# Kernel optimization log

Measured on AMD Instinct MI355X. Metric: run time of the kernel, lower is better.

## Reference

```python
import jax, jax.numpy as jnp
import numpy as np

B, L, D, Z, V, N, MAXPOS = 8, 2048, 1024, 128, 2048, 16, 2048


def setup_inputs():
    key = jax.random.key(0)
    ks = jax.random.split(key, 16)
    std = 0.02
    return {
        "x": jax.random.normal(ks[0], (B, L, D), jnp.float32),
        "norm1_w": jnp.ones((D,), jnp.float32),
        "norm1_b": jnp.zeros((D,), jnp.float32),
        "ema_delta": jax.random.normal(ks[1], (D, N), jnp.float32) * 0.2,
        "ema_alpha": jax.random.normal(ks[2], (D, N), jnp.float32) * 0.2,
        "ema_beta": jax.random.normal(ks[3], (D, N), jnp.float32) * 0.02,
        "ema_gamma": jax.random.normal(ks[4], (D, N), jnp.float32),
        "ema_omega": jax.random.normal(ks[5], (D,), jnp.float32),
        "vproj_w": jax.random.normal(ks[6], (D, V), jnp.float32) * std,
        "vproj_b": jnp.zeros((V,), jnp.float32),
        "mx_w": jax.random.normal(ks[7], (D, Z + V + 2 * D), jnp.float32) * std,
        "mx_b": jnp.zeros((Z + V + 2 * D,), jnp.float32),
        "h_w": jax.random.normal(ks[8], (V, D), jnp.float32) * std,
        "h_b": jnp.zeros((D,), jnp.float32),
        "att_gamma": jax.random.normal(ks[9], (2, Z), jnp.float32) * std,
        "att_beta": jnp.zeros((2, Z), jnp.float32),
        "rel_bias": jax.random.normal(ks[10], (2 * MAXPOS - 1,), jnp.float32) * std,
        "norm2_w": jnp.ones((D,), jnp.float32),
        "norm2_b": jnp.zeros((D,), jnp.float32),
        "ff_w1": jax.random.normal(ks[11], (D, 2 * D), jnp.float32) * std,
        "ff_b1": jnp.zeros((2 * D,), jnp.float32),
        "ff_w2": jax.random.normal(ks[12], (2 * D, D), jnp.float32) * std,
        "ff_b2": jnp.zeros((D,), jnp.float32),
    }


def _layernorm(x, w, b):
    mu = jnp.mean(x, -1, keepdims=True)
    var = jnp.mean((x - mu) ** 2, -1, keepdims=True)
    return (x - mu) * jax.lax.rsqrt(var + 1e-5) * w + b


def reference(x, norm1_w, norm1_b, ema_delta, ema_alpha, ema_beta, ema_gamma, ema_omega,
              vproj_w, vproj_b, mx_w, mx_b, h_w, h_b, att_gamma, att_beta, rel_bias,
              norm2_w, norm2_b, ff_w1, ff_b1, ff_w2, ff_b2):
    residual = x
    xn = _layernorm(x, norm1_w, norm1_b)                       # prenorm
    v = jax.nn.silu(xn @ vproj_w + vproj_b)                    # (B L V)

    # --- MultiHeadEMA (damped EMA state space) via FFT convolution ---
    p = jax.nn.sigmoid(ema_delta)                              # (D N)
    q = 1.0 - p * jax.nn.sigmoid(ema_alpha)                    # (D N) in (0,1)
    t = jnp.arange(L, dtype=jnp.float32)
    vander = jnp.exp(t[None, None, :] * jnp.log(q)[:, :, None])       # (D N L)
    kern = jnp.einsum('dnl,dn->dl', (p * ema_beta)[:, :, None] * vander,
                      ema_gamma * np.float32(1.0 / np.sqrt(N)))        # (D L)
    xT = jnp.swapaxes(xn, 1, 2)                                # (B D L)
    k_f = jnp.fft.rfft(kern, n=2 * L)
    x_f = jnp.fft.rfft(xT, n=2 * L)
    ema = jnp.fft.irfft(x_f * k_f, n=2 * L)[..., :L]           # causal conv
    mx = jax.nn.silu(jnp.swapaxes(ema, 1, 2) + xn * ema_omega) # (B L D)

    # --- moving-average gated attention ---
    base = mx @ mx_w + mx_b                                    # (B L D+Z+V+D)
    u, zr, hx = jnp.split(base, [D, D + Z + V], axis=-1)
    u = jax.nn.sigmoid(u)                                      # update gate
    zr = jax.nn.silu(zr)
    z, r = zr[..., :Z], zr[..., Z:]                            # (B L Z), (B L V)
    zqk = z[:, :, None, :] * att_gamma + att_beta              # (B L 2 Z)
    qh, kh = zqk[:, :, 0, :], zqk[:, :, 1, :]

    # simple relative positional bias: Toeplitz bias[i,j] = b[L-1 + j - i]
    bseg = rel_bias[MAXPOS - L:MAXPOS + L - 1]                 # (2L-1,)
    idx = (L - 1) + jnp.arange(L)[None, :] - jnp.arange(L)[:, None]
    bias = bseg[idx]                                           # (L L)

    qk = jnp.einsum('blz,bmz->blm', qh * np.float32(Z ** -0.5), kh) + bias
    attn = jax.nn.softmax(qk, axis=-1)                         # (B L L)
    h = jnp.einsum('blm,bmv->blv', attn, v)                    # (B L V)
    h = jax.nn.silu(hx + (h * r) @ h_w + h_b)                  # (B L D)
    out = residual + u * (h - residual)                        # addcmul gate

    # --- prenorm FFN residual block (expand=2, silu) ---
    y = _layernorm(out, norm2_w, norm2_b)
    y = jax.nn.silu(y @ ff_w1 + ff_b1) @ ff_w2 + ff_b2
    return out + y
```

## Files before the change

kernel.cpp:

```cpp
#include <hip/hip_runtime.h>
#include <hip/hip_bf16.h>
#include <cstdint>

#define B_ 8
#define L_ 2048
#define D_ 1024
#define Z_ 128
#define V_ 2048
#define N_ 16
#define NC_ 16
#define CL_ 128

typedef unsigned short ushort_t;
typedef __attribute__((ext_vector_type(8))) short short8;
typedef __attribute__((ext_vector_type(4))) float floatx4;

__device__ __forceinline__ float b2f(ushort_t u){ union{float f;unsigned i;}x; x.i=((unsigned)u)<<16; return x.f; }
__device__ __forceinline__ ushort_t f2b(float f){ union{float f;unsigned i;}x; x.f=f; unsigned r=(x.i+0x7fffu+((x.i>>16)&1u))>>16; return (ushort_t)r; }
__device__ __forceinline__ float sigmoidf_(float x){ return 1.0f/(1.0f+__expf(-x)); }
__device__ __forceinline__ float siluf_(float x){ return x/(1.0f+__expf(-x)); }

#define GLL16(g,l) __builtin_amdgcn_global_load_lds( \
    (const __attribute__((address_space(1))) void*)(g), \
    (__attribute__((address_space(3))) void*)(l), 16, 0, 0)

__device__ __forceinline__ float blockSum(float v){
  #pragma unroll
  for(int off=32;off;off>>=1) v += __shfl_xor(v,off);
  __shared__ float sm[4];
  __syncthreads();
  if((threadIdx.x&63)==0) sm[threadIdx.x>>6]=v;
  __syncthreads();
  return (sm[0]+sm[1])+(sm[2]+sm[3]);
}
__device__ __forceinline__ float blockMax(float v){
  #pragma unroll
  for(int off=32;off;off>>=1) v = fmaxf(v,__shfl_xor(v,off));
  __shared__ float sm[4];
  __syncthreads();
  if((threadIdx.x&63)==0) sm[threadIdx.x>>6]=v;
  __syncthreads();
  return fmaxf(fmaxf(sm[0],sm[1]),fmaxf(sm[2],sm[3]));
}

__global__ __launch_bounds__(256) void ln_kernel(const float* __restrict__ in,
    const float* __restrict__ w, const float* __restrict__ b,
    ushort_t* __restrict__ o16){
  const int row = blockIdx.x;
  const int t = threadIdx.x;
  const float* p = in + (size_t)row*D_;
  float4 v = *reinterpret_cast<const float4*>(p + t*4);
  float s = (v.x+v.y)+(v.z+v.w);
  s = blockSum(s);
  float mu = s*(1.0f/D_);
  float dx=v.x-mu, dy=v.y-mu, dz=v.z-mu, dw=v.w-mu;
  float ss = dx*dx+dy*dy+dz*dz+dw*dw;
  ss = blockSum(ss);
  float inv = rsqrtf(ss*(1.0f/D_)+1e-5f);
  float4 wv = *reinterpret_cast<const float4*>(w + t*4);
  float4 bv = *reinterpret_cast<const float4*>(b + t*4);
  union{ushort_t u[4]; uint2 q;} o;
  o.u[0]=f2b(dx*inv*wv.x+bv.x); o.u[1]=f2b(dy*inv*wv.y+bv.y);
  o.u[2]=f2b(dz*inv*wv.z+bv.z); o.u[3]=f2b(dw*inv*wv.w+bv.w);
  *reinterpret_cast<uint2*>(o16+(size_t)row*D_+t*4)=o.q;
}

__global__ __launch_bounds__(256) void transpose_all(
    const float* __restrict__ vproj_w, ushort_t* __restrict__ wvT,
    const float* __restrict__ mx_w,    ushort_t* __restrict__ wmxT,
    const float* __restrict__ h_w,     ushort_t* __restrict__ whT,
    const float* __restrict__ ff_w1,   ushort_t* __restrict__ wf1T,
    const float* __restrict__ ff_w2,   ushort_t* __restrict__ wf2T){
  const float* in; ushort_t* out; int R, C;
  switch(blockIdx.z){
    case 0: in=vproj_w; out=wvT;  R=D_;   C=V_;   break;
    case 1: in=mx_w;    out=wmxT; R=D_;   C=4224; break;
    case 2: in=h_w;     out=whT;  R=V_;   C=D_;   break;
    case 3: in=ff_w1;   out=wf1T; R=D_;   C=2*D_; break;
    default:in=ff_w2;   out=wf2T; R=2*D_; C=D_;   break;
  }
  int bx=blockIdx.x*32, by=blockIdx.y*32;
  if(bx>=C || by>=R) return;
  __shared__ float tile[32][33];
  int tx=threadIdx.x&31, ty=threadIdx.x>>5;
  #pragma unroll
  for(int i=0;i<32;i+=8) tile[ty+i][tx] = in[(size_t)(by+ty+i)*C + bx+tx];
  __syncthreads();
  #pragma unroll
  for(int i=0;i<32;i+=8) out[(size_t)(bx+ty+i)*R + by+tx] = f2b(tile[tx][ty+i]);
}

__global__ __launch_bounds__(256) void ema_setup(const float* __restrict__ delta,
    const float* __restrict__ alpha, const float* __restrict__ beta,
    const float* __restrict__ gamma, float* __restrict__ qarr,
    float* __restrict__ warr, float* __restrict__ qC){
  int i = blockIdx.x*256+threadIdx.x;
  if(i>=D_*N_) return;
  float p = sigmoidf_(delta[i]);
  float q = 1.0f - p*sigmoidf_(alpha[i]);
  qarr[i]=q; warr[i]=p*beta[i]*gamma[i]*0.25f;
  qC[i]=powf(q,(float)CL_);
}

__global__ __launch_bounds__(256) void ema_pass1(const ushort_t* __restrict__ xn,
    const float* __restrict__ qarr, float* __restrict__ E){
  int idx = blockIdx.x*256+threadIdx.x;
  int d = idx & (D_-1); int c = (idx>>10)&15; int b = idx>>14;
  const ushort_t* xp = xn + ((size_t)b*L_ + c*CL_)*D_ + d;
  float q[N_], s[N_];
  #pragma unroll
  for(int n=0;n<N_;n++){ q[n]=qarr[d*N_+n]; s[n]=0.0f; }
  for(int i=0;i<CL_;i+=8){
    float xv[8];
    #pragma unroll
    for(int j=0;j<8;j++) xv[j]=b2f(xp[(size_t)(i+j)*D_]);
    #pragma unroll
    for(int j=0;j<8;j++){
      #pragma unroll
      for(int n=0;n<N_;n++) s[n]=fmaf(q[n],s[n],xv[j]);
    }
  }
  float* Ep = E + (((size_t)b*NC_+c)*N_)*D_ + d;
  #pragma unroll
  for(int n=0;n<N_;n++) Ep[(size_t)n*D_]=s[n];
}

__global__ __launch_bounds__(256) void ema_pass2(const float* __restrict__ E,
    const float* __restrict__ qC, float* __restrict__ In){
  int idx = blockIdx.x*256+threadIdx.x;
  int d = idx & (D_-1); int b = idx>>10;
  float S[N_], qc[N_];
  #pragma unroll
  for(int n=0;n<N_;n++){ S[n]=0.0f; qc[n]=qC[d*N_+n]; }
  for(int c=0;c<NC_;c++){
    size_t base = (((size_t)b*NC_+c)*N_)*D_ + d;
    #pragma unroll
    for(int n=0;n<N_;n++) In[base+(size_t)n*D_]=S[n];
    #pragma unroll
    for(int n=0;n<N_;n++) S[n]=fmaf(qc[n],S[n],E[base+(size_t)n*D_]);
  }
}

__global__ __launch_bounds__(256) void ema_pass3_mx(const ushort_t* __restrict__ xn,
    const float* __restrict__ qarr, const float* __restrict__ warr,
    const float* __restrict__ In, const float* __restrict__ omega,
    ushort_t* __restrict__ mx){
  int idx = blockIdx.x*256+threadIdx.x;
  int d = idx & (D_-1); int c = (idx>>10)&15; int b = idx>>14;
  const ushort_t* xp = xn + ((size_t)b*L_ + c*CL_)*D_ + d;
  ushort_t* op = mx + ((size_t)b*L_ + c*CL_)*D_ + d;
  size_t base = (((size_t)b*NC_+c)*N_)*D_ + d;
  float om = omega[d];
  float q[N_], w[N_], s[N_];
  #pragma unroll
  for(int n=0;n<N_;n++){ q[n]=qarr[d*N_+n]; w[n]=warr[d*N_+n]; s[n]=In[base+(size_t)n*D_]; }
  for(int i=0;i<CL_;i+=8){
    float xv[8];
    #pragma unroll
    for(int j=0;j<8;j++) xv[j]=b2f(xp[(size_t)(i+j)*D_]);
    #pragma unroll
    for(int j=0;j<8;j++){
      float a=0.0f;
      #pragma unroll
      for(int n=0;n<N_;n++){ s[n]=fmaf(q[n],s[n],xv[j]); a=fmaf(w[n],s[n],a); }
      op[(size_t)(i+j)*D_]=f2b(siluf_(a + xv[j]*om));
    }
  }
}

__global__ __launch_bounds__(256) void softmax_kernel(const float* __restrict__ qk,
    ushort_t* __restrict__ attn){
  size_t row = blockIdx.x;
  const float* p = qk + row*(size_t)L_;
  int t = threadIdx.x;
  float vals[8];
  #pragma unroll
  for(int i=0;i<8;i++) vals[i]=p[i*256+t];
  float m=-__builtin_inff();
  #pragma unroll
  for(int i=0;i<8;i++) m=fmaxf(m,vals[i]);
  m = blockMax(m);
  float s=0.0f;
  #pragma unroll
  for(int i=0;i<8;i++){ vals[i]=__expf(vals[i]-m); s+=vals[i]; }
  s = blockSum(s);
  float inv = 1.0f/s;
  ushort_t* q = attn + row*(size_t)L_;
  #pragma unroll
  for(int i=0;i<8;i++) q[i*256+t]=f2b(vals[i]*inv);
}

#define BAR() __builtin_amdgcn_s_barrier()
#define VMW(n) asm volatile("s_waitcnt vmcnt(" #n ")" ::: "memory")
#define BAR_ACQ(vm) do{ \
    asm volatile("s_waitcnt vmcnt(" #vm ")" ::: "memory"); \
    __builtin_amdgcn_s_barrier(); }while(0)
#define BAR_REL() do{ \
    asm volatile("" ::: "memory"); \
    __builtin_amdgcn_s_barrier(); \
    asm volatile("" ::: "memory"); }while(0)

template<class Epi>
__global__ __launch_bounds__(256) void gemm_nt(const ushort_t* __restrict__ A,
    const ushort_t* __restrict__ B, int M, int N, int K, Epi epi){
  __shared__ __align__(16) ushort_t As[2][128*64];
  __shared__ __align__(16) ushort_t Bs[2][128*64];
  const int t = threadIdx.x;
  const int wave=t>>6, lane=t&63, quad=lane>>4, l16=lane&15;
  const int bm=blockIdx.x*128, bn=blockIdx.y*128;
  const int wm=(wave>>1)*64, wn=(wave&1)*64;
  const int srow = wave*32 + (lane>>3);
  const int schk = ((lane&7) ^ (lane>>3)) * 8;
  const ushort_t* gA[4]; const ushort_t* gB[4];
  ushort_t *lA[4], *lB[4];
  #pragma unroll
  for(int i=0;i<4;i++){
    gA[i] = A + (size_t)(bm+srow+i*8)*K + schk;
    gB[i] = B + (size_t)(bn+srow+i*8)*K + schk;
    lA[i] = &As[0][(wave*32+i*8)*64];
    lB[i] = &Bs[0][(wave*32+i*8)*64];
  }
  const ushort_t* ra[2][4]; const ushort_t* rb[2][4];
  #pragma unroll
  for(int h=0;h<2;h++)
    #pragma unroll
    for(int i=0;i<4;i++){
      int rrA = wm+i*16+l16, rrB = wn+i*16+l16;
      ra[h][i] = &As[0][rrA*64 + (((h*4+quad)^(rrA&7))*8)];
      rb[h][i] = &Bs[0][rrB*64 + (((h*4+quad)^(rrB&7))*8)];
    }
  floatx4 acc[4][4];
  #pragma unroll
  for(int i=0;i<4;i++)
    #pragma unroll
    for(int j=0;j<4;j++) acc[i][j]=(floatx4){0.f,0.f,0.f,0.f};

  const int nk = K>>6;
  #pragma unroll
  for(int i=0;i<4;i++){ GLL16(gA[i], lA[i]); GLL16(gB[i], lB[i]); }

  for(int t0=0;t0<nk;t0+=2){
    {
      const int k0=(t0+1)<<6;
      #pragma unroll
      for(int i=0;i<4;i++){ GLL16(gA[i]+k0, lA[i]+(128*64)); GLL16(gB[i]+k0, lB[i]+(128*64)); }
    }
    BAR_ACQ(8);
    #pragma unroll
    for(int h=0;h<2;h++){
      short8 af[4], bf[4];
      #pragma unroll
      for(int mt=0;mt<4;mt++) af[mt]=*reinterpret_cast<const short8*>(ra[h][mt]);
      #pragma unroll
      for(int nt=0;nt<4;nt++) bf[nt]=*reinterpret_cast<const short8*>(rb[h][nt]);
      #pragma unroll
      for(int mt=0;mt<4;mt++)
        #pragma unroll
        for(int nt=0;nt<4;nt++)
          acc[mt][nt]=__builtin_amdgcn_mfma_f32_16x16x32_bf16(af[mt],bf[nt],acc[mt][nt],0,0,0);
    }
    BAR_REL();
    if(t0+2<nk){
      const int k0=(t0+2)<<6;
      #pragma unroll
      for(int i=0;i<4;i++){ GLL16(gA[i]+k0, lA[i]); GLL16(gB[i]+k0, lB[i]); }
      BAR_ACQ(8);
    } else {
      BAR_ACQ(0);
    }
    #pragma unroll
    for(int h=0;h<2;h++){
      short8 af[4], bf[4];
      #pragma unroll
      for(int mt=0;mt<4;mt++) af[mt]=*reinterpret_cast<const short8*>(ra[h][mt]+(128*64));
      #pragma unroll
      for(int nt=0;nt<4;nt++) bf[nt]=*reinterpret_cast<const short8*>(rb[h][nt]+(128*64));
      #pragma unroll
      for(int mt=0;mt<4;mt++)
        #pragma unroll
        for(int nt=0;nt<4;nt++)
          acc[mt][nt]=__builtin_amdgcn_mfma_f32_16x16x32_bf16(af[mt],bf[nt],acc[mt][nt],0,0,0);
    }
    BAR_REL();
  }

  #pragma unroll
  for(int mt=0;mt<4;mt++)
    #pragma unroll
    for(int nt=0;nt<4;nt++)
      #pragma unroll
      for(int r=0;r<4;r++){
        int row=bm+wm+mt*16+quad*4+r;
        int col=bn+wn+nt*16+l16;
        epi(acc[mt][nt][r], row, col, 0);
      }
}

#define RA4(buf,kh,mh) \
  af[0]=pA8[(buf)*2048+(kh)*1024+((mh)*4+0)*64+rowA]; \
  af[1]=pA8[(buf)*2048+(kh)*1024+((mh)*4+1)*64+rowA]; \
  af[2]=pA8[(buf)*2048+(kh)*1024+((mh)*4+2)*64+rowA]; \
  af[3]=pA8[(buf)*2048+(kh)*1024+((mh)*4+3)*64+rowA];
#define RB4(buf,kh) \
  bf[0]=pB8[(buf)*2048+(kh)*1024+0*64+rowB]; \
  bf[1]=pB8[(buf)*2048+(kh)*1024+1*64+rowB]; \
  bf[2]=pB8[(buf)*2048+(kh)*1024+2*64+rowB]; \
  bf[3]=pB8[(buf)*2048+(kh)*1024+3*64+rowB];
#define MMA16(mh) \
  __builtin_amdgcn_s_setprio(1); \
  acc[(mh)*4+0][0]=__builtin_amdgcn_mfma_f32_16x16x32_bf16(af[0],bf[0],acc[(mh)*4+0][0],0,0,0); \
  acc[(mh)*4+0][1]=__builtin_amdgcn_mfma_f32_16x16x32_bf16(af[0],bf[1],acc[(mh)*4+0][1],0,0,0); \
  acc[(mh)*4+0][2]=__builtin_amdgcn_mfma_f32_16x16x32_bf16(af[0],bf[2],acc[(mh)*4+0][2],0,0,0); \
  acc[(mh)*4+0][3]=__builtin_amdgcn_mfma_f32_16x16x32_bf16(af[0],bf[3],acc[(mh)*4+0][3],0,0,0); \
  acc[(mh)*4+1][0]=__builtin_amdgcn_mfma_f32_16x16x32_bf16(af[1],bf[0],acc[(mh)*4+1][0],0,0,0); \
  acc[(mh)*4+1][1]=__builtin_amdgcn_mfma_f32_16x16x32_bf16(af[1],bf[1],acc[(mh)*4+1][1],0,0,0); \
  acc[(mh)*4+1][2]=__builtin_amdgcn_mfma_f32_16x16x32_bf16(af[1],bf[2],acc[(mh)*4+1][2],0,0,0); \
  acc[(mh)*4+1][3]=__builtin_amdgcn_mfma_f32_16x16x32_bf16(af[1],bf[3],acc[(mh)*4+1][3],0,0,0); \
  acc[(mh)*4+2][0]=__builtin_amdgcn_mfma_f32_16x16x32_bf16(af[2],bf[0],acc[(mh)*4+2][0],0,0,0); \
  acc[(mh)*4+2][1]=__builtin_amdgcn_mfma_f32_16x16x32_bf16(af[2],bf[1],acc[(mh)*4+2][1],0,0,0); \
  acc[(mh)*4+2][2]=__builtin_amdgcn_mfma_f32_16x16x32_bf16(af[2],bf[2],acc[(mh)*4+2][2],0,0,0); \
  acc[(mh)*4+2][3]=__builtin_amdgcn_mfma_f32_16x16x32_bf16(af[2],bf[3],acc[(mh)*4+2][3],0,0,0); \
  acc[(mh)*4+3][0]=__builtin_amdgcn_mfma_f32_16x16x32_bf16(af[3],bf[0],acc[(mh)*4+3][0],0,0,0); \
  acc[(mh)*4+3][1]=__builtin_amdgcn_mfma_f32_16x16x32_bf16(af[3],bf[1],acc[(mh)*4+3][1],0,0,0); \
  acc[(mh)*4+3][2]=__builtin_amdgcn_mfma_f32_16x16x32_bf16(af[3],bf[2],acc[(mh)*4+3][2],0,0,0); \
  acc[(mh)*4+3][3]=__builtin_amdgcn_mfma_f32_16x16x32_bf16(af[3],bf[3],acc[(mh)*4+3][3],0,0,0); \
  __builtin_amdgcn_s_setprio(0);
#define SA2(b,kh,k0) \
  GLL16(gA0+(k0)+(kh)*32, lAd+((b)*2+(kh))*8192); \
  GLL16(gA1+(k0)+(kh)*32, lAd+((b)*2+(kh))*8192+512);
#define SB2(b,kh,k0) \
  GLL16(gB0+(k0)+(kh)*32, lBd+((b)*2+(kh))*8192); \
  GLL16(gB1+(k0)+(kh)*32, lBd+((b)*2+(kh))*8192+512);

#define TILE_S(buf,k1) { \
  short8 af[4], bf[4]; \
  RA4(buf,0,0) RB4(buf,0) \
  SA2((buf)^1,0,k1) \
  BAR(); MMA16(0) BAR(); \
  RA4(buf,0,1) \
  SB2((buf)^1,0,k1) \
  BAR(); MMA16(1) VMW(4); BAR(); \
  RA4(buf,1,0) RB4(buf,1) \
  SA2((buf)^1,1,k1) \
  BAR(); MMA16(0) BAR(); \
  RA4(buf,1,1) \
  SB2((buf)^1,1,k1) \
  BAR(); MMA16(1) VMW(4); BAR(); \
}
#define TILE_E(buf) { \
  short8 af[4], bf[4]; \
  RA4(buf,0,0) RB4(buf,0) \
  BAR(); MMA16(0) BAR(); \
  RA4(buf,0,1) \
  BAR(); MMA16(1) VMW(0); BAR(); \
  RA4(buf,1,0) RB4(buf,1) \
  BAR(); MMA16(0) BAR(); \
  RA4(buf,1,1) \
  BAR(); MMA16(1) \
}

template<class Epi>
__global__ __launch_bounds__(512) void gemm_nt2(const ushort_t* __restrict__ A0,
    const ushort_t* __restrict__ B0, int M, int N, int K,
    size_t za, size_t zb, Epi epi){
  __shared__ __align__(16) ushort_t As[2*2*8192];
  __shared__ __align__(16) ushort_t Bs[2*2*8192];
  const int t = threadIdx.x;
  const int wave=t>>6, lane=t&63, quad=lane>>4, l16=lane&15;
  int bx, by;
  {
    int gx=gridDim.x, gy=gridDim.y;
    int f = blockIdx.y*gx + blockIdx.x;
    if((gy==4 || gy==8) && (gx%(32/gy))==0){
      int GW = 32/gy, nst = gx/GW;
      int s, r;
      if((nst&7)==0){ int xc=f&7; int j=f>>3; s = xc*(nst>>3) + (j>>5); r = j&31; }
      else { s = f>>5; r = f&31; }
      bx = s*GW + (r%GW); by = r/GW;
    } else { bx = blockIdx.x; by = blockIdx.y; }
  }
  const int z = blockIdx.z;
  const ushort_t* A = A0 + (size_t)z*za;
  const ushort_t* B = B0 + (size_t)z*zb;
  const int bm=bx*256, bn=by*256;
  const int wm=(wave>>2)*128, wn=(wave&3)*64;
  const int g8 = ((lane&3) ^ ((lane>>3)&3))*8;
  const ushort_t* gA0 = A + (size_t)(bm + wave*32 + (lane>>2))*K + g8;
  const ushort_t* gA1 = gA0 + (size_t)16*K;
  const ushort_t* gB0 = B + (size_t)(bn + wave*32 + (lane>>2))*K + g8;
  const ushort_t* gB1 = gB0 + (size_t)16*K;
  ushort_t* lAd = As + wave*1024;
  ushort_t* lBd = Bs + wave*1024;
  const short8* pA8 = reinterpret_cast<const short8*>(As);
  const short8* pB8 = reinterpret_cast<const short8*>(Bs);
  const int swl = (l16>>1)&3;
  const int rowA = (wm+l16)*4 + (quad^swl);
  const int rowB = (wn+l16)*4 + (quad^swl);
  floatx4 acc[8][4];
  #pragma unroll
  for(int i=0;i<8;i++)
    #pragma unroll
    for(int j=0;j<4;j++) acc[i][j]=(floatx4){0.f,0.f,0.f,0.f};

  const int nkt = K>>6;
  SA2(0,0,0) SB2(0,0,0) SA2(0,1,0) SB2(0,1,0)
  VMW(4); BAR();

  for(int t0=0; t0+2<nkt; t0+=2){
    TILE_S(0,(t0+1)<<6)
    TILE_S(1,(t0+2)<<6)
  }
  TILE_S(0,(nkt-1)<<6)
  TILE_E(1)

  #pragma unroll
  for(int mt=0;mt<8;mt++)
    #pragma unroll
    for(int nt=0;nt<4;nt++)
      #pragma unroll
      for(int r=0;r<4;r++){
        int row=bm+wm+mt*16+quad*4+r;
        int col=bn+wn+nt*16+l16;
        epi(acc[mt][nt][r], row, col, z);
      }
}

struct EpiV {
  ushort_t* vT; const float* vb;
  __device__ void operator()(float v,int row,int col,int) const {
    float s = siluf_(v + vb[col]);
    int b = row>>11, l = row&(L_-1);
    vT[((size_t)b*V_ + col)*L_ + l] = f2b(s);
  }
};
struct EpiU {
  ushort_t* u; const float* mxb;
  __device__ void operator()(float v,int row,int col,int) const {
    u[(size_t)row*D_+col]=f2b(sigmoidf_(v+mxb[col]));
  }
};
struct EpiQKh {
  ushort_t* qh; ushort_t* kh; const float* mxb; const float* ag; const float* ab;
  __device__ void operator()(float v,int row,int col,int) const {
    float z=siluf_(v+mxb[col]);
    qh[(size_t)row*Z_+col]=f2b(z*ag[col]+ab[col]);
    kh[(size_t)row*Z_+col]=f2b(z*ag[Z_+col]+ab[Z_+col]);
  }
};
struct EpiR {
  ushort_t* r; const float* mxb;
  __device__ void operator()(float v,int row,int col,int) const {
    r[(size_t)row*V_+col]=f2b(siluf_(v+mxb[col]));
  }
};
struct EpiHx {
  ushort_t* hx; const float* mxb;
  __device__ void operator()(float v,int row,int col,int) const {
    hx[(size_t)row*D_+col]=f2b(v+mxb[col]);
  }
};
struct EpiQK {
  float* qk; const float* rb;
  __device__ void operator()(float v,int row,int col,int) const {
    qk[(size_t)row*L_+col] = v*0.08838834764831845f + rb[L_-1+col-row];
  }
};
struct EpiH {
  ushort_t* hr; const ushort_t* r;
  __device__ void operator()(float v,int row,int col,int z) const {
    size_t idx = ((size_t)z*L_ + row)*V_ + col;
    hr[idx] = f2b(v * b2f(r[idx]));
  }
};
struct EpiOut {
  float* out; const float* x; const ushort_t* u; const ushort_t* hx; const float* hb;
  __device__ void operator()(float v,int row,int col,int) const {
    size_t idx=(size_t)row*D_+col;
    float h2 = siluf_(b2f(hx[idx]) + v + hb[col]);
    float xv = x[idx];
    out[idx] = xv + b2f(u[idx])*(h2-xv);
  }
};
struct EpiF1 {
  ushort_t* f1; const float* b1;
  __device__ void operator()(float v,int row,int col,int) const {
    f1[(size_t)row*(2*D_)+col]=f2b(siluf_(v+b1[col]));
  }
};
struct EpiFinal {
  float* dout; const float* b2;
  __device__ void operator()(float v,int row,int col,int) const {
    size_t idx=(size_t)row*D_+col;
    dout[idx] = dout[idx] + v + b2[col];
  }
};

extern "C" void kernel_launch(void* const* d_in, const int* in_sizes, int n_in,
                              void* d_out, int out_size, void* d_ws, size_t ws_size,
                              hipStream_t stream){
  const float* x        = (const float*)d_in[0];
  const float* norm1_w  = (const float*)d_in[1];
  const float* norm1_b  = (const float*)d_in[2];
  const float* ema_delta= (const float*)d_in[3];
  const float* ema_alpha= (const float*)d_in[4];
  const float* ema_beta = (const float*)d_in[5];
  const float* ema_gamma= (const float*)d_in[6];
  const float* ema_omega= (const float*)d_in[7];
  const float* vproj_w  = (const float*)d_in[8];
  const float* vproj_b  = (const float*)d_in[9];
  const float* mx_w     = (const float*)d_in[10];
  const float* mx_b     = (const float*)d_in[11];
  const float* h_w      = (const float*)d_in[12];
  const float* h_b      = (const float*)d_in[13];
  const float* att_gamma= (const float*)d_in[14];
  const float* att_beta = (const float*)d_in[15];
  const float* rel_bias = (const float*)d_in[16];
  const float* norm2_w  = (const float*)d_in[17];
  const float* norm2_b  = (const float*)d_in[18];
  const float* ff_w1    = (const float*)d_in[19];
  const float* ff_b1    = (const float*)d_in[20];
  const float* ff_w2    = (const float*)d_in[21];
  const float* ff_b2    = (const float*)d_in[22];
  float* dout = (float*)d_out;
  char* ws = (char*)d_ws;

  size_t cur = 0;
  auto take = [&](size_t b)->size_t{ size_t o=cur; cur += (b+255)&~255ull; return o; };
  const size_t o_wvT  = take((size_t)V_*D_*2);
  const size_t o_wmxT = take((size_t)4224*D_*2);
  const size_t o_whT  = take((size_t)D_*V_*2);
  const size_t o_wf1T = take((size_t)2*D_*D_*2);
  const size_t o_wf2T = take((size_t)D_*2*D_*2);
  const size_t o_qarr = take((size_t)D_*N_*4);
  const size_t o_warr = take((size_t)D_*N_*4);
  const size_t o_qC   = take((size_t)D_*N_*4);
  const size_t globals_end = cur;

  int g = 0;
  size_t o_xn=0,o_mx=0,o_u=0,o_hx=0,o_r=0,o_qh=0,o_kh=0,o_qk=0,o_at=0;
  for(int cand=8; cand>=1; cand>>=1){
    cur = globals_end;
    size_t xn_o = take((size_t)cand*L_*D_*2);
    size_t mx_o = take((size_t)cand*L_*D_*2);
    size_t u_o  = take((size_t)cand*L_*D_*2);
    size_t hx_o = take((size_t)cand*L_*D_*2);
    size_t r_o  = take((size_t)cand*L_*V_*2);
    size_t qh_o = take((size_t)cand*L_*Z_*2);
    size_t kh_o = take((size_t)cand*L_*Z_*2);
    size_t qk_o, at_o;
    if(cand>=4){ qk_o = xn_o; at_o = xn_o + (size_t)L_*L_*4; }
    else { qk_o = take((size_t)L_*L_*4); at_o = take((size_t)L_*L_*2); }
    if(cur <= ws_size){
      g=cand; o_xn=xn_o; o_mx=mx_o; o_u=u_o; o_hx=hx_o; o_r=r_o;
      o_qh=qh_o; o_kh=kh_o; o_qk=qk_o; o_at=at_o; break;
    }
  }
  if(!g) return;

  ushort_t* wvT  = (ushort_t*)(ws+o_wvT);
  ushort_t* wmxT = (ushort_t*)(ws+o_wmxT);
  ushort_t* whT  = (ushort_t*)(ws+o_whT);
  ushort_t* wf1T = (ushort_t*)(ws+o_wf1T);
  ushort_t* wf2T = (ushort_t*)(ws+o_wf2T);
  float* qarr = (float*)(ws+o_qarr);
  float* warr = (float*)(ws+o_warr);
  float* qC   = (float*)(ws+o_qC);
  ushort_t* xn  = (ushort_t*)(ws+o_xn);
  ushort_t* mx  = (ushort_t*)(ws+o_mx);
  ushort_t* u16 = (ushort_t*)(ws+o_u);
  ushort_t* hx16= (ushort_t*)(ws+o_hx);
  ushort_t* r16 = (ushort_t*)(ws+o_r);
  ushort_t* qh  = (ushort_t*)(ws+o_qh);
  ushort_t* kh  = (ushort_t*)(ws+o_kh);
  float*    qk  = (float*)   (ws+o_qk);
  ushort_t* attn= (ushort_t*)(ws+o_at);
  float*    E   = (float*)(ws+o_u);
  float*    In  = (float*)(ws+o_hx);
  ushort_t* ybf = xn;
  ushort_t* f1  = r16;

  int nbat; ushort_t* attnB;
  if(g>=4){ nbat = g/2; attnB = mx; }
  else    { nbat = 1;   attnB = attn; }

  transpose_all<<<dim3(132, 64, 5), 256, 0, stream>>>(
      vproj_w, wvT, mx_w, wmxT, h_w, whT, ff_w1, wf1T, ff_w2, wf2T);
  ema_setup<<<(D_*N_)/256, 256, 0, stream>>>(ema_delta, ema_alpha, ema_beta, ema_gamma, qarr, warr, qC);

  for(int gi=0; gi<B_/g; ++gi){
    const int RG = g*L_;
    const float* x_g  = x    + (size_t)gi*RG*D_;
    float*       do_g = dout + (size_t)gi*RG*D_;
    ushort_t*    vT   = (ushort_t*)do_g;

    ln_kernel<<<RG, 256, 0, stream>>>(x_g, norm1_w, norm1_b, xn);
    ema_pass1<<<(g*NC_*D_)/256, 256, 0, stream>>>(xn, qarr, E);
    ema_pass2<<<(g*D_)/256, 256, 0, stream>>>(E, qC, In);
    ema_pass3_mx<<<(g*NC_*D_)/256, 256, 0, stream>>>(xn, qarr, warr, In, ema_omega, mx);

    { EpiV e{vT, vproj_b};
      gemm_nt2<<<dim3(RG/256, V_/256), 512, 0, stream>>>(xn, wvT, RG, V_, D_, 0, 0, e); }

    { EpiU e{u16, mx_b};
      gemm_nt2<<<dim3(RG/256, D_/256), 512, 0, stream>>>(mx, wmxT, RG, D_, D_, 0, 0, e); }
    { EpiQKh e{qh, kh, mx_b+D_, att_gamma, att_beta};
      gemm_nt<<<dim3(RG/128, Z_/128), 256, 0, stream>>>(mx, wmxT+(size_t)D_*D_, RG, Z_, D_, e); }
    { EpiR e{r16, mx_b+D_+Z_};
      gemm_nt2<<<dim3(RG/256, V_/256), 512, 0, stream>>>(mx, wmxT+(size_t)(D_+Z_)*D_, RG, V_, D_, 0, 0, e); }
    { EpiHx e{hx16, mx_b+D_+Z_+V_};
      gemm_nt2<<<dim3(RG/256, D_/256), 512, 0, stream>>>(mx, wmxT+(size_t)(D_+Z_+V_)*D_, RG, D_, D_, 0, 0, e); }

    for(int q0=0; q0<g; q0+=nbat){
      for(int bi=q0; bi<q0+nbat; ++bi){
        { EpiQK e{qk, rel_bias};
          gemm_nt<<<dim3(L_/128, L_/128), 256, 0, stream>>>(
            qh+(size_t)bi*L_*Z_, kh+(size_t)bi*L_*Z_, L_, L_, Z_, e); }
        softmax_kernel<<<L_, 256, 0, stream>>>(qk, attnB+(size_t)(bi-q0)*L_*L_);
      }
      { EpiH e{r16+(size_t)q0*L_*V_, r16+(size_t)q0*L_*V_};
        gemm_nt2<<<dim3(L_/256, V_/256, nbat), 512, 0, stream>>>(
          attnB, vT+(size_t)q0*V_*L_, L_, V_, L_,
          (size_t)L_*L_, (size_t)V_*L_, e); }
    }

    { EpiOut e{do_g, x_g, u16, hx16, h_b};
      gemm_nt2<<<dim3(RG/256, D_/256), 512, 0, stream>>>(r16, whT, RG, D_, V_, 0, 0, e); }
    ln_kernel<<<RG, 256, 0, stream>>>(do_g, norm2_w, norm2_b, ybf);
    { EpiF1 e{f1, ff_b1};
      gemm_nt2<<<dim3(RG/256, (2*D_)/256), 512, 0, stream>>>(ybf, wf1T, RG, 2*D_, D_, 0, 0, e); }
    { EpiFinal e{do_g, ff_b2};
      gemm_nt2<<<dim3(RG/256, D_/256), 512, 0, stream>>>(f1, wf2T, RG, D_, 2*D_, 0, 0, e); }
  }
}
```

Baseline: 1.286 ms.

## Replace double-buffered LDS pipeline with single-buffer half-tile staging in gemm_nt2

The 256x256 GEMM kernel drops its double-buffered LDS (halving shared memory) and instead computes each K half-tile from a single buffer, then reloads that half after a barrier. This cuts LDS usage, which could allow more resident blocks and fewer barriers inside the MFMA stream. The trade-off is that global-to-LDS loads no longer overlap with MFMA work on the same block, so latency has to be hidden by other blocks or waves.

```diff
diff --git a/kernel.cpp b/kernel.cpp
--- a/kernel.cpp
+++ b/kernel.cpp
@@ -296,16 +296,17 @@
       }
 }
 
-#define RA4(buf,kh,mh) \
-  af[0]=pA8[(buf)*2048+(kh)*1024+((mh)*4+0)*64+rowA]; \
-  af[1]=pA8[(buf)*2048+(kh)*1024+((mh)*4+1)*64+rowA]; \
-  af[2]=pA8[(buf)*2048+(kh)*1024+((mh)*4+2)*64+rowA]; \
-  af[3]=pA8[(buf)*2048+(kh)*1024+((mh)*4+3)*64+rowA];
-#define RB4(buf,kh) \
-  bf[0]=pB8[(buf)*2048+(kh)*1024+0*64+rowB]; \
-  bf[1]=pB8[(buf)*2048+(kh)*1024+1*64+rowB]; \
-  bf[2]=pB8[(buf)*2048+(kh)*1024+2*64+rowB]; \
-  bf[3]=pB8[(buf)*2048+(kh)*1024+3*64+rowB];
+
+#define RA6(kh,mh) \
+  af[0]=pA8[(kh)*1024+((mh)*4+0)*64+rowA]; \
+  af[1]=pA8[(kh)*1024+((mh)*4+1)*64+rowA]; \
+  af[2]=pA8[(kh)*1024+((mh)*4+2)*64+rowA]; \
+  af[3]=pA8[(kh)*1024+((mh)*4+3)*64+rowA];
+#define RB6(kh) \
+  bf[0]=pB8[(kh)*1024+0*64+rowB]; \
+  bf[1]=pB8[(kh)*1024+1*64+rowB]; \
+  bf[2]=pB8[(kh)*1024+2*64+rowB]; \
+  bf[3]=pB8[(kh)*1024+3*64+rowB];
 #define MMA16(mh) \
   __builtin_amdgcn_s_setprio(1); \
   acc[(mh)*4+0][0]=__builtin_amdgcn_mfma_f32_16x16x32_bf16(af[0],bf[0],acc[(mh)*4+0][0],0,0,0); \
@@ -325,46 +326,41 @@
   acc[(mh)*4+3][2]=__builtin_amdgcn_mfma_f32_16x16x32_bf16(af[3],bf[2],acc[(mh)*4+3][2],0,0,0); \
   acc[(mh)*4+3][3]=__builtin_amdgcn_mfma_f32_16x16x32_bf16(af[3],bf[3],acc[(mh)*4+3][3],0,0,0); \
   __builtin_amdgcn_s_setprio(0);
-#define SA2(b,kh,k0) \
-  GLL16(gA0+(k0)+(kh)*32, lAd+((b)*2+(kh))*8192); \
-  GLL16(gA1+(k0)+(kh)*32, lAd+((b)*2+(kh))*8192+512);
-#define SB2(b,kh,k0) \
-  GLL16(gB0+(k0)+(kh)*32, lBd+((b)*2+(kh))*8192); \
-  GLL16(gB1+(k0)+(kh)*32, lBd+((b)*2+(kh))*8192+512);
-
-#define TILE_S(buf,k1) { \
+#define SA6(kh,k0) \
+  GLL16(gA0+(k0)+(kh)*32, lAd+(kh)*8192); \
+  GLL16(gA1+(k0)+(kh)*32, lAd+(kh)*8192+512);
+#define SB6(kh,k0) \
+  GLL16(gB0+(k0)+(kh)*32, lBd+(kh)*8192); \
+  GLL16(gB1+(k0)+(kh)*32, lBd+(kh)*8192+512);
+
+#define TILE_S6(k1) { \
   short8 af[4], bf[4]; \
-  RA4(buf,0,0) RB4(buf,0) \
-  SA2((buf)^1,0,k1) \
-  BAR(); MMA16(0) BAR(); \
-  RA4(buf,0,1) \
-  SB2((buf)^1,0,k1) \
-  BAR(); MMA16(1) VMW(4); BAR(); \
-  RA4(buf,1,0) RB4(buf,1) \
-  SA2((buf)^1,1,k1) \
-  BAR(); MMA16(0) BAR(); \
-  RA4(buf,1,1) \
-  SB2((buf)^1,1,k1) \
-  BAR(); MMA16(1) VMW(4); BAR(); \
-}
-#define TILE_E(buf) { \
+  RA6(0,0) RB6(0) MMA16(0) \
+  RA6(0,1) MMA16(1) \
+  BAR(); \
+  SA6(0,k1) SB6(0,k1) \
+  VMW(4); BAR(); \
+  RA6(1,0) RB6(1) MMA16(0) \
+  RA6(1,1) MMA16(1) \
+  BAR(); \
+  SA6(1,k1) SB6(1,k1) \
+  VMW(4); BAR(); \
+}
+#define TILE_E6() { \
   short8 af[4], bf[4]; \
-  RA4(buf,0,0) RB4(buf,0) \
-  BAR(); MMA16(0) BAR(); \
-  RA4(buf,0,1) \
-  BAR(); MMA16(1) VMW(0); BAR(); \
-  RA4(buf,1,0) RB4(buf,1) \
-  BAR(); MMA16(0) BAR(); \
-  RA4(buf,1,1) \
-  BAR(); MMA16(1) \
+  RA6(0,0) RB6(0) MMA16(0) \
+  RA6(0,1) MMA16(1) \
+  VMW(0); BAR(); \
+  RA6(1,0) RB6(1) MMA16(0) \
+  RA6(1,1) MMA16(1) \
 }
 
 template<class Epi>
 __global__ __launch_bounds__(512) void gemm_nt2(const ushort_t* __restrict__ A0,
     const ushort_t* __restrict__ B0, int M, int N, int K,
     size_t za, size_t zb, Epi epi){
-  __shared__ __align__(16) ushort_t As[2*2*8192];
-  __shared__ __align__(16) ushort_t Bs[2*2*8192];
+  __shared__ __align__(16) ushort_t As[2*8192];
+  __shared__ __align__(16) ushort_t Bs[2*8192];
   const int t = threadIdx.x;
   const int wave=t>>6, lane=t&63, quad=lane>>4, l16=lane&15;
   int bx, by;
@@ -403,15 +399,13 @@
     for(int j=0;j<4;j++) acc[i][j]=(floatx4){0.f,0.f,0.f,0.f};
 
   const int nkt = K>>6;
-  SA2(0,0,0) SB2(0,0,0) SA2(0,1,0) SB2(0,1,0)
+  SA6(0,0) SB6(0,0) SA6(1,0) SB6(1,0)
   VMW(4); BAR();
 
-  for(int t0=0; t0+2<nkt; t0+=2){
-    TILE_S(0,(t0+1)<<6)
-    TILE_S(1,(t0+2)<<6)
-  }
-  TILE_S(0,(nkt-1)<<6)
-  TILE_E(1)
+  for(int t0=0; t0<nkt-1; ++t0){
+    TILE_S6((t0+1)<<6)
+  }
+  TILE_E6()
 
   #pragma unroll
   for(int mt=0;mt<8;mt++)
```

Measured after the change: 1.378 ms. 1.07x slower.
